# Performance work log

Measured on AMD Instinct MI355X. Metric: run time of the kernel, lower is better.

Reference implementation:

```python
import jax, jax.numpy as jnp
import numpy as np

B, S, IN_DIM, LATENT, SYM = 16, 256, 512, 512, 128
NUM_NODES, NUM_CODES, MAX_OPS, MAX_BUS = 4, 512, 4, 32
HALT_EPS, MAX_SEQ = 1e-3, 256


def setup_inputs() -> dict:
    key = jax.random.key(0)
    ks = jax.random.split(key, 10)

    def lin(k, out_d, in_d, pre=()):
        kw, kb = jax.random.split(k)
        lim = 1.0 / np.sqrt(in_d).astype(np.float32)
        w = jax.random.uniform(kw, pre + (out_d, in_d), minval=-lim, maxval=lim, dtype=jnp.float32)
        b = jax.random.uniform(kb, pre + (out_d,), minval=-lim, maxval=lim, dtype=jnp.float32)
        return w, b

    x = jax.random.normal(ks[0], (B, S, IN_DIM), jnp.float32)
    ipw, ipb = lin(ks[1], LATENT, IN_DIM)
    tp = jax.random.normal(ks[2], (1, MAX_SEQ, LATENT), jnp.float32)
    N = (NUM_NODES,)
    sw, sb = lin(ks[3], SYM, LATENT, N)
    qw, qb = lin(ks[4], 1, SYM, N)
    rw, rb = lin(ks[5], LATENT, 2 * LATENT, N)
    c1w, c1b = lin(ks[6], LATENT, LATENT + SYM, N)
    c2w, c2b = lin(ks[7], LATENT, LATENT, N)
    cb = jax.random.normal(ks[8], (NUM_NODES, NUM_CODES, SYM), jnp.float32)
    return {"x": x, "input_proj_w": ipw, "input_proj_b": ipb, "token_prompts": tp,
            "sym_w": sw, "sym_b": sb, "qry_w": qw, "qry_b": qb,
            "read_w": rw, "read_b": rb, "c1_w": c1w, "c1_b": c1b,
            "c2_w": c2w, "c2_b": c2b, "codebook": cb}


def _forward(x, input_proj_w, input_proj_b, token_prompts, sym_w, sym_b, qry_w, qry_b,
             read_w, read_b, c1_w, c1_b, c2_w, c2_b, codebook):
    Bx, Sx, _ = x.shape
    N = Bx * Sx
    # input projection + positional prompts
    out = jnp.einsum('bsi,li->bsl', x, input_proj_w) + input_proj_b + token_prompts[:, :Sx, :]
    prev_out = out
    active = jnp.ones((Bx, Sx), bool)
    token_tags = jnp.zeros((Bx, Sx, SYM), x.dtype)
    # TensorBus rolling buffers ([max_bus, B, S, dim]); with default cfg the roll branch never fires
    sym_buf = jnp.zeros((MAX_BUS, Bx, Sx, SYM), x.dtype)          # slot 0 = zero tags (initial append)
    out_buf = jnp.zeros((MAX_BUS, Bx, Sx, LATENT), x.dtype).at[0].set(out)
    msg_mask = jnp.zeros((MAX_BUS,), bool).at[0].set(True)
    ptr = 1  # static python int: appends are a fixed unrolled schedule (1 + MAX_OPS*NUM_NODES <= MAX_BUS)
    slot_ids = jnp.arange(MAX_BUS)

    for t in range(MAX_OPS):
        # snapshot of active messages for this op step (get_active)
        snap_active = msg_mask & (slot_ids < ptr)                  # [MAX_BUS]
        syms_flat = sym_buf.reshape(MAX_BUS, N, SYM)
        outs_flat = out_buf.reshape(MAX_BUS, N, LATENT)
        keep_all = jnp.ones((MAX_BUS,), bool)
        for n in range(NUM_NODES):
            # relevance of each bus message per token; inactive slots masked out of argmax
            rel = jnp.einsum('tnd,d->tn', syms_flat, qry_w[n, 0]) + qry_b[n, 0]
            rel = jnp.where(snap_active[:, None], rel, jnp.asarray(-1e9, rel.dtype))
            top = jnp.argmax(rel, axis=0)                          # [N] chosen message per token
            chosen = jnp.take_along_axis(outs_flat, top[None, :, None], axis=0)[0]  # [N, LATENT]
            bus_ctx = chosen.reshape(Bx, Sx, LATENT)
            z = jnp.concatenate([out, bus_ctx], axis=-1)
            z_read = jnp.einsum('bsk,lk->bsl', z, read_w[n]) + read_b[n]
            raw_sym = jnp.einsum('bsl,dl->bsd', z_read, sym_w[n]) + sym_b[n]
            # EMA quantizer (eval): nearest codebook entry by euclidean distance
            flat = raw_sym.reshape(-1, SYM)
            cbn = codebook[n]
            d2 = (jnp.sum(flat * flat, axis=-1, keepdims=True)
                  - 2.0 * flat @ cbn.T + jnp.sum(cbn * cbn, axis=-1))
            idx = jnp.argmin(d2, axis=-1)
            quant = cbn[idx].reshape(Bx, Sx, SYM)
            h = jnp.concatenate([z_read, quant], axis=-1)
            hid = jax.nn.relu(jnp.einsum('bsk,lk->bsl', h, c1_w[n]) + c1_b[n])
            node_out = jnp.einsum('bsl,ol->bso', hid, c2_w[n]) + c2_b[n] + out
            # halting / selective update
            delta = jnp.linalg.norm(node_out - prev_out, axis=-1)
            halt = (delta < HALT_EPS) & active
            assigned = active if t > 0 else jnp.ones_like(active)
            upd = assigned & jnp.logical_not(halt)
            out = jnp.where(upd[..., None], node_out, out)
            token_tags = jnp.where(upd[..., None], quant, token_tags)
            # bus.append
            sym_buf = sym_buf.at[ptr].set(quant)
            out_buf = out_buf.at[ptr].set(node_out)
            msg_mask = msg_mask.at[ptr].set(True)
            ptr += 1
            # keep_mask: messages never selected by any token stay alive
            counts = jnp.zeros((MAX_BUS,), jnp.int32).at[top].add(1)
            keep_all = keep_all & (counts == 0)
            active = active & jnp.logical_not(halt)
            prev_out = out
        # mark_consumed: ones over valid slots ANDed with per-node keep masks at snapshot-active
        # slots (inactive/new slots get True -> faithful to the torch init_global_mask quirk)
        msg_mask = (slot_ids < ptr) & keep_all
    return out


def reference(x, input_proj_w, input_proj_b, token_prompts, sym_w, sym_b, qry_w, qry_b,
              read_w, read_b, c1_w, c1_b, c2_w, c2_b, codebook):
    return _forward(x, input_proj_w, input_proj_b, token_prompts, sym_w, sym_b, qry_w, qry_b,
                    read_w, read_b, c1_w, c1_b, c2_w, c2_b, codebook)
```

## Files before the change

### kernel.cpp

```cpp
#include <hip/hip_runtime.h>
#include <math.h>

namespace {

typedef _Float16 f16;
typedef __attribute__((ext_vector_type(8))) _Float16 f16x8;
typedef __attribute__((ext_vector_type(4))) float f32x4;

constexpr int TOK = 4096;
constexpr int DL  = 512;
constexpr int DS  = 128;
constexpr int NC  = 512;
constexpr int NSLOT = 13;

__device__ __forceinline__ float wsum(float v){
  #pragma unroll
  for(int o=32;o>0;o>>=1) v += __shfl_xor(v,o);
  return v;
}

__device__ __forceinline__ void gload16(const void* g, void* l){
  __builtin_amdgcn_global_load_lds(
      (const __attribute__((address_space(1))) unsigned int*)g,
      (__attribute__((address_space(3))) unsigned int*)l, 16, 0, 0);
}

__device__ __forceinline__ int slotb(int row, int g){
  return (((row ^ ((row>>2)&1))<<2) | (g ^ (row&3))) << 4;
}

template<int AMODE,int EPI>
__global__ __launch_bounds__(256,2) void mgemm(
    const f16* __restrict__ A1h, const f16* __restrict__ A1l,
    const f16* __restrict__ A2h, const f16* __restrict__ A2l,
    const int* __restrict__ gidx,
    const f16* __restrict__ Bh, const f16* __restrict__ Bl,
    const float* __restrict__ bias, const float* __restrict__ res,
    float* __restrict__ Cf, f16* __restrict__ Ch, f16* __restrict__ Cl,
    f16* __restrict__ C2h, f16* __restrict__ C2l,
    int K, int K0)
{
  constexpr int SMB = 16384;
  __shared__ __align__(16) char smem[2*SMB];
  const int tid = threadIdx.x, w = tid>>6, l = tid&63;
  const int m0 = blockIdx.x*64, n0 = blockIdx.y*64;
  const int NK = K>>5, SW = K0>>5;

  const f16* sp[4]; const f16* sp2[4]; int loff[4];
  #pragma unroll
  for(int i=0;i<4;i++){
    int c = 4*w+i;
    int isA = (c<8);
    int plane = isA ? (c>>2) : ((c-8)>>2);
    int cidx  = isA ? (c&3)  : ((c-8)&3);
    loff[i] = (isA?0:8192) + plane*4096 + cidx*1024;
    int s = (cidx<<6) + l;
    int rp = s>>2, row = rp ^ ((rp>>2)&1), g = (s&3) ^ (row&3);
    int g8 = g<<3;
    if(isA){
      int m = m0 + row;
      const f16* p1 = (plane? A1l : A1h) + ((size_t)m<<9) + g8;
      sp[i] = p1;
      if(AMODE==1)      sp2[i] = (plane? A2l : A2h) + ((size_t)gidx[m]<<21) + ((size_t)m<<9) + g8;
      else if(AMODE==2) sp2[i] = (plane? A2l : A2h) + ((size_t)gidx[m]<<7) + g8;
      else              sp2[i] = p1;
    } else {
      sp[i] = (plane? Bl : Bh) + (size_t)(n0+row)*K + g8;
      sp2[i] = sp[i];
    }
  }

  const int wr = w>>1, wc = w&1, q = l>>4, r = l&15;
  int aoff[2], boff[2];
  #pragma unroll
  for(int i=0;i<2;i++) aoff[i] = slotb(32*wr + 16*i + r, q);
  #pragma unroll
  for(int j=0;j<2;j++) boff[j] = 8192 + slotb(32*wc + 16*j + r, q);

  f32x4 acc1[2][2] = {}, acc2[2][2] = {};

  #pragma unroll
  for(int i=0;i<4;i++) gload16(sp[i], smem + loff[i]);
  __syncthreads();

  int buf = 0;
  for(int kt=0; kt<NK; ++kt){
    if(kt+1 < NK){
      int nb = buf^1;
      #pragma unroll
      for(int i=0;i<4;i++){
        if(AMODE!=0 && (4*w+i)<8 && (kt+1)==SW) sp[i] = sp2[i];
        else                                     sp[i] += 32;
        gload16(sp[i], smem + nb*SMB + loff[i]);
      }
    }
    const char* Lb = smem + buf*SMB;
    f16x8 ah[2], al[2], bh[2], bl[2];
    #pragma unroll
    for(int i=0;i<2;i++){
      ah[i] = *(const f16x8*)(Lb + aoff[i]);
      al[i] = *(const f16x8*)(Lb + 4096 + aoff[i]);
    }
    #pragma unroll
    for(int j=0;j<2;j++){
      bh[j] = *(const f16x8*)(Lb + boff[j]);
      bl[j] = *(const f16x8*)(Lb + 4096 + boff[j]);
    }
    #pragma unroll
    for(int i=0;i<2;i++)
      #pragma unroll
      for(int j=0;j<2;j++){
        acc1[i][j] = __builtin_amdgcn_mfma_f32_16x16x32_f16(ah[i], bh[j], acc1[i][j], 0,0,0);
        acc2[i][j] = __builtin_amdgcn_mfma_f32_16x16x32_f16(ah[i], bl[j], acc2[i][j], 0,0,0);
        acc2[i][j] = __builtin_amdgcn_mfma_f32_16x16x32_f16(al[i], bh[j], acc2[i][j], 0,0,0);
      }
    __syncthreads();
    buf ^= 1;
  }

  #pragma unroll
  for(int i=0;i<2;i++)
    #pragma unroll
    for(int j=0;j<2;j++)
      #pragma unroll
      for(int rr=0;rr<4;rr++){
        int rowm = m0 + 32*wr + 16*i + 4*q + rr;
        int coln = n0 + 32*wc + 16*j + r;
        size_t o = ((size_t)rowm<<9) + coln;
        float v = acc1[i][j][rr] + acc2[i][j][rr]*(1.0f/2048.0f) + bias[coln];
        if(EPI==2) v = fmaxf(v, 0.f);
        if(EPI==3) v += res[o];
        if(EPI==4) v += res[(((size_t)(rowm&255))<<9) + coln];
        if(EPI==1 || EPI==3 || EPI==4) Cf[o] = v;
        if(EPI==0 || EPI==2 || EPI==4){
          f16 h = (f16)v;
          Ch[o] = h; Cl[o] = (f16)((v-(float)h)*2048.0f);
        }
        if(EPI==4){
          f16 h = (f16)v;
          C2h[o] = h; C2l[o] = (f16)((v-(float)h)*2048.0f);
        }
      }
}

__global__ void split_k(const float* __restrict__ src, f16* __restrict__ hi,
                        f16* __restrict__ lo, int n){
  for(int i = blockIdx.x*256 + threadIdx.x; i < n; i += gridDim.x*256){
    float v = src[i];
    f16 h = (f16)v;
    hi[i] = h;
    lo[i] = (f16)((v - (float)h)*2048.0f);
  }
}

__global__ __launch_bounds__(256)
void wcomb_k(const float* __restrict__ A, const float* __restrict__ Wall,
             float* __restrict__ C)
{
  constexpr int T=256;
  __shared__ float As[32][68];
  __shared__ float Ws[32][132];
  const int tid = threadIdx.x;
  const int m0 = blockIdx.x*64, n0 = blockIdx.y*128;
  const float* W = Wall + (size_t)(m0>>9)*DS*DL;
  const int ty = tid>>4, tx = tid&15;
  float4 pa[2], pw[4];
  auto loadA = [&](int k0){
    #pragma unroll
    for(int it=0; it<2; ++it){
      int v = tid + T*it; int rr = v>>3, c4 = v&7;
      pa[it] = *(const float4*)(A + (size_t)(m0+rr)*DS + k0 + (c4<<2));
    }
  };
  auto loadW = [&](int k0){
    #pragma unroll
    for(int it=0; it<4; ++it){
      int v = tid + T*it; int rr = v>>5, c4 = v&31;
      pw[it] = *(const float4*)(W + (size_t)(k0+rr)*DL + n0 + (c4<<2));
    }
  };
  float acc[4][8];
  #pragma unroll
  for(int i=0;i<4;i++)
    #pragma unroll
    for(int j=0;j<8;j++) acc[i][j]=0.f;
  loadA(0); loadW(0);
  for(int k0=0; k0<DS; k0+=32){
    __syncthreads();
    #pragma unroll
    for(int it=0; it<2; ++it){
      int v = tid + T*it; int rr=v>>3, c4=v&7;
      As[(c4<<2)+0][rr]=pa[it].x; As[(c4<<2)+1][rr]=pa[it].y;
      As[(c4<<2)+2][rr]=pa[it].z; As[(c4<<2)+3][rr]=pa[it].w;
    }
    #pragma unroll
    for(int it=0; it<4; ++it){
      int v = tid + T*it; int rr=v>>5, c4=v&31;
      *(float4*)&Ws[rr][c4<<2] = pw[it];
    }
    __syncthreads();
    if(k0+32 < DS){ loadA(k0+32); loadW(k0+32); }
    #pragma unroll
    for(int kk=0; kk<32; kk++){
      float4 a4 = *(const float4*)&As[kk][ty<<2];
      float4 b0 = *(const float4*)&Ws[kk][tx<<2];
      float4 b1 = *(const float4*)&Ws[kk][64+(tx<<2)];
      float a[4]={a4.x,a4.y,a4.z,a4.w};
      float b[8]={b0.x,b0.y,b0.z,b0.w,b1.x,b1.y,b1.z,b1.w};
      #pragma unroll
      for(int i=0;i<4;i++)
        #pragma unroll
        for(int j=0;j<8;j++) acc[i][j] = fmaf(a[i], b[j], acc[i][j]);
    }
  }
  #pragma unroll
  for(int i=0;i<4;i++){
    int m = m0 + (ty<<2) + i;
    #pragma unroll
    for(int j=0;j<8;j++){
      int n = n0 + ((j<4)? (tx<<2)+j : 64+(tx<<2)+(j-4));
      C[((size_t)m<<9)+n] = acc[i][j];
    }
  }
}

__global__ void init_k(int* __restrict__ msg, int* __restrict__ act,
                       float* __restrict__ relc, const float* __restrict__ qb,
                       int* __restrict__ cons){
  int i = blockIdx.x*256 + threadIdx.x;
  if(i < TOK){
    act[i] = 1;
    #pragma unroll
    for(int nn=0;nn<4;nn++) relc[nn*TOK + i] = qb[nn];
  }
  if(i < 32){ msg[i] = (i==0) ? 1 : 0; cons[i] = 0; }
}

__global__ void bias2_k(const float* __restrict__ cb, const float* __restrict__ sb,
                        float* __restrict__ b2){
  int row = blockIdx.x*4 + (threadIdx.x>>6);
  int lane = threadIdx.x&63;
  const float* cv = cb + ((size_t)row<<7);
  const float* sbn = sb + ((row>>9)<<7);
  float c0=cv[lane], c1=cv[lane+64];
  float nrm = c0*c0 + c1*c1;
  float dt  = c0*sbn[lane] + c1*sbn[lane+64];
  nrm = wsum(nrm); dt = wsum(dt);
  if(lane==0) b2[row] = dt - 0.5f*nrm;
}

__global__ void relmax_k(const float* __restrict__ relc, const int* __restrict__ msg,
                         int pt, int node, int* __restrict__ top, int* __restrict__ cons){
  int tok = blockIdx.x*256 + threadIdx.x;
  float best = -1e9f; int bs = 0;
  for(int s=0;s<pt;s++){
    float v = msg[s] ? relc[(size_t)((s<<2)+node)*TOK + tok] : -1e9f;
    if(v > best){ best = v; bs = s; }
  }
  top[tok] = bs;
  cons[bs] = 1;
}

__global__ void codemax_k(const float* __restrict__ sc, int* __restrict__ idx){
  int m = blockIdx.x*4 + (threadIdx.x>>6);
  int lane = threadIdx.x&63;
  const float* row = sc + ((size_t)m<<9);
  float best = -INFINITY; int bi = 0;
  #pragma unroll
  for(int rr=0;rr<8;rr++){
    int c = lane + (rr<<6);
    float v = row[c];
    if(v > best){ best=v; bi=c; }
  }
  #pragma unroll
  for(int o=32;o>0;o>>=1){
    float ov = __shfl_xor(best,o);
    int   oi = __shfl_xor(bi,o);
    if(ov > best || (ov==best && oi<bi)){ best=ov; bi=oi; }
  }
  if(lane==0) idx[m]=bi;
}

__global__ void mupdate_k(const float* __restrict__ no_, float* __restrict__ out,
                          f16* __restrict__ outh, f16* __restrict__ outl,
                          f16* __restrict__ slabh, f16* __restrict__ slabl,
                          float* __restrict__ relc, const int* __restrict__ idx,
                          const float* __restrict__ cbn, const float* __restrict__ qw,
                          const float* __restrict__ qb, int* __restrict__ act,
                          int* __restrict__ cons, int* __restrict__ msg,
                          int t, int ptr, int pe){
  int m = blockIdx.x*4 + (threadIdx.x>>6);
  int lane = threadIdx.x&63;
  const float* nrow = no_ + ((size_t)m<<9);
  float* orow = out + ((size_t)m<<9);
  float nv[8]; float s=0.f;
  #pragma unroll
  for(int rr=0;rr<8;rr++){
    int c = lane + (rr<<6);
    nv[rr]=nrow[c];
    float d = nv[rr]-orow[c]; s += d*d;
  }
  s = wsum(s);
  float delta = sqrtf(s);
  int a = act[m];
  int halt = (delta < 1e-3f) && a;
  int assigned = (t>0) ? a : 1;
  int upd = assigned && !halt;
  if(lane==0) act[m] = a && !halt;
  if(upd){
    #pragma unroll
    for(int rr=0;rr<8;rr++){
      int c = lane + (rr<<6);
      float v = nv[rr];
      orow[c] = v;
      f16 h = (f16)v;
      outh[((size_t)m<<9)+c] = h;
      outl[((size_t)m<<9)+c] = (f16)((v-(float)h)*2048.0f);
    }
  }
  if(ptr >= 0){
    size_t so = (((size_t)ptr)<<21) + ((size_t)m<<9);
    #pragma unroll
    for(int rr=0;rr<8;rr++){
      int c = lane + (rr<<6);
      float v = nv[rr];
      f16 h = (f16)v;
      slabh[so+c] = h;
      slabl[so+c] = (f16)((v-(float)h)*2048.0f);
    }
    const float* qv = cbn + ((size_t)idx[m]<<7);
    float q0=qv[lane], q1=qv[lane+64];
    #pragma unroll
    for(int nn=0;nn<4;nn++){
      float pr = q0*qw[(nn<<7)+lane] + q1*qw[(nn<<7)+64+lane];
      pr = wsum(pr);
      if(lane==0) relc[(size_t)((ptr<<2)+nn)*TOK + m] = pr + qb[nn];
    }
  }
  if(pe >= 0 && blockIdx.x==0 && threadIdx.x < 32){
    int s2 = threadIdx.x;
    msg[s2] = (s2 < pe) && !cons[s2];
    cons[s2] = 0;
  }
}

}

extern "C" void kernel_launch(void* const* d_in, const int* in_sizes, int n_in,
                              void* d_out, int out_size, void* d_ws, size_t ws_size,
                              hipStream_t stream)
{
  (void)in_sizes; (void)n_in; (void)out_size; (void)ws_size;
  const float* x   = (const float*)d_in[0];
  const float* ipw = (const float*)d_in[1];
  const float* ipb = (const float*)d_in[2];
  const float* tp  = (const float*)d_in[3];
  const float* sw  = (const float*)d_in[4];
  const float* sb  = (const float*)d_in[5];
  const float* qw  = (const float*)d_in[6];
  const float* qb  = (const float*)d_in[7];
  const float* rw  = (const float*)d_in[8];
  const float* rb  = (const float*)d_in[9];
  const float* c1w = (const float*)d_in[10];
  const float* c1b = (const float*)d_in[11];
  const float* c2w = (const float*)d_in[12];
  const float* c2b = (const float*)d_in[13];
  const float* cb  = (const float*)d_in[14];
  float* out = (float*)d_out;

  char* p = (char*)d_ws;
  auto alloc = [&](size_t b)->char*{ char* r=p; p += (b+255)&~(size_t)255; return r; };
  f16* slabh = (f16*)alloc((size_t)NSLOT*TOK*DL*2);
  f16* slabl = (f16*)alloc((size_t)NSLOT*TOK*DL*2);
  f16* outh  = (f16*)alloc((size_t)TOK*DL*2);
  f16* outl  = (f16*)alloc((size_t)TOK*DL*2);
  f16* zh    = (f16*)alloc((size_t)TOK*DL*2);
  f16* zl    = (f16*)alloc((size_t)TOK*DL*2);
  f16* hh    = (f16*)alloc((size_t)TOK*DL*2);
  f16* hl    = (f16*)alloc((size_t)TOK*DL*2);
  float* sn  = (float*)alloc((size_t)TOK*DL*4);
  f16* rwh   = (f16*)alloc((size_t)4*DL*1024*2);
  f16* rwl   = (f16*)alloc((size_t)4*DL*1024*2);
  f16* c1h   = (f16*)alloc((size_t)4*DL*640*2);
  f16* c1l   = (f16*)alloc((size_t)4*DL*640*2);
  f16* c2h   = (f16*)alloc((size_t)4*DL*DL*2);
  f16* c2l   = (f16*)alloc((size_t)4*DL*DL*2);
  f16* wch   = (f16*)alloc((size_t)4*NC*DL*2);
  f16* wcl   = (f16*)alloc((size_t)4*NC*DL*2);
  f16* iph   = (f16*)alloc((size_t)DL*DL*2);
  f16* ipl   = (f16*)alloc((size_t)DL*DL*2);
  f16* cbh   = (f16*)alloc((size_t)4*NC*DS*2);
  f16* cbl   = (f16*)alloc((size_t)4*NC*DS*2);
  float* b2  = (float*)alloc(4*NC*4);
  float* relc= (float*)alloc((size_t)NSLOT*4*TOK*4);
  int* top   = (int*)alloc(TOK*4);
  int* idxb  = (int*)alloc(TOK*4);
  int* act   = (int*)alloc(TOK*4);
  int* msg   = (int*)alloc(256);
  int* cons  = (int*)alloc(256);

  dim3 G(64,8), B(256);

  init_k<<<16,256,0,stream>>>(msg, act, relc, qb, cons);
  bias2_k<<<512,256,0,stream>>>(cb, sb, b2);
  wcomb_k<<<dim3(32,4),B,0,stream>>>(cb, sw, sn);
  split_k<<<2048,256,0,stream>>>(x,   hh,  hl,  TOK*DL);
  split_k<<<512 ,256,0,stream>>>(ipw, iph, ipl, DL*DL);
  split_k<<<2048,256,0,stream>>>(rw,  rwh, rwl, 4*DL*1024);
  split_k<<<2048,256,0,stream>>>(c1w, c1h, c1l, 4*DL*640);
  split_k<<<1024,256,0,stream>>>(c2w, c2h, c2l, 4*DL*DL);
  split_k<<<512 ,256,0,stream>>>(cb,  cbh, cbl, 4*NC*DS);
  split_k<<<1024,256,0,stream>>>(sn,  wch, wcl, 4*NC*DL);

  mgemm<0,4><<<G,B,0,stream>>>(hh,hl, nullptr,nullptr, nullptr, iph,ipl,
      ipb, tp, out, outh,outl, slabh,slabl, DL, DL);

  int ptr = 1;
  for(int t=0;t<4;t++){
    int pt = 1 + 4*t;
    for(int n=0;n<4;n++){
      relmax_k<<<16,256,0,stream>>>(relc, msg, pt, n, top, cons);
      mgemm<1,0><<<G,B,0,stream>>>(outh,outl, slabh,slabl, top,
          rwh+(size_t)n*DL*1024, rwl+(size_t)n*DL*1024, rb+(size_t)n*DL,
          nullptr, nullptr, zh,zl, nullptr,nullptr, 1024, 512);
      mgemm<0,1><<<G,B,0,stream>>>(zh,zl, nullptr,nullptr, nullptr,
          wch+(size_t)n*NC*DL, wcl+(size_t)n*NC*DL, b2+(size_t)n*NC,
          nullptr, sn, nullptr,nullptr, nullptr,nullptr, 512, 512);
      codemax_k<<<1024,256,0,stream>>>(sn, idxb);
      mgemm<2,2><<<G,B,0,stream>>>(zh,zl, cbh+(size_t)n*NC*DS, cbl+(size_t)n*NC*DS, idxb,
          c1h+(size_t)n*DL*640, c1l+(size_t)n*DL*640, c1b+(size_t)n*DL,
          nullptr, nullptr, hh,hl, nullptr,nullptr, 640, 512);
      mgemm<0,3><<<G,B,0,stream>>>(hh,hl, nullptr,nullptr, nullptr,
          c2h+(size_t)n*DL*DL, c2l+(size_t)n*DL*DL, c2b+(size_t)n*DL,
          out, sn, nullptr,nullptr, nullptr,nullptr, 512, 512);
      mupdate_k<<<1024,256,0,stream>>>(sn, out, outh,outl, slabh,slabl, relc, idxb,
          cb+(size_t)n*NC*DS, qw, qb, act, cons, msg, t,
          (t<3)? ptr : -1, (n==3 && t<3)? (1+4*(t+1)) : -1);
      ptr++;
    }
  }
}
```

Baseline: 1.321 ms.

## Fuse codebook argmax into score GEMM epilogue and triple-buffer GEMM loads

The score GEMM no longer writes the full 4096x512 fp32 score matrix. Its epilogue now reduces each 64-column tile to a per-row partial argmax, and the following c1 GEMM combines the eight partials into the final code index. This removes the separate codemax kernel and the score matrix round trip through memory. Separately, the GEMM mainloop moves from double to triple buffering with explicit vmcnt waits, so loads stay two tiles ahead. That triples LDS to 48KB per block, which may lower occupancy under launch_bounds(256,2).

```diff
diff --git a/kernel.cpp b/kernel.cpp
--- a/kernel.cpp
+++ b/kernel.cpp
@@ -38,13 +38,32 @@
     const float* __restrict__ bias, const float* __restrict__ res,
     float* __restrict__ Cf, f16* __restrict__ Ch, f16* __restrict__ Cl,
     f16* __restrict__ C2h, f16* __restrict__ C2l,
+    float* __restrict__ scpv, int* __restrict__ scpi, int* __restrict__ idxg,
     int K, int K0)
 {
   constexpr int SMB = 16384;
-  __shared__ __align__(16) char smem[2*SMB];
+  __shared__ __align__(16) char smem[3*SMB];
+  __shared__ int gsel[64];
+  __shared__ float redv[4][32];
+  __shared__ int   redi[4][32];
   const int tid = threadIdx.x, w = tid>>6, l = tid&63;
   const int m0 = blockIdx.x*64, n0 = blockIdx.y*64;
   const int NK = K>>5, SW = K0>>5;
+
+  if(AMODE==2){
+    if(tid<64){
+      int m = m0+tid;
+      float bv = -INFINITY; int bi = 0;
+      #pragma unroll
+      for(int y=0;y<8;y++){
+        float v = scpv[(size_t)y*TOK + m];
+        if(v > bv){ bv=v; bi=scpi[(size_t)y*TOK + m]; }
+      }
+      gsel[tid]=bi;
+      idxg[m]=bi;
+    }
+    __syncthreads();
+  }
 
   const f16* sp[4]; const f16* sp2[4]; int loff[4];
   #pragma unroll
@@ -62,7 +81,7 @@
       const f16* p1 = (plane? A1l : A1h) + ((size_t)m<<9) + g8;
       sp[i] = p1;
       if(AMODE==1)      sp2[i] = (plane? A2l : A2h) + ((size_t)gidx[m]<<21) + ((size_t)m<<9) + g8;
-      else if(AMODE==2) sp2[i] = (plane? A2l : A2h) + ((size_t)gidx[m]<<7) + g8;
+      else if(AMODE==2) sp2[i] = (plane? A2l : A2h) + ((size_t)gsel[row]<<7) + g8;
       else              sp2[i] = p1;
     } else {
       sp[i] = (plane? Bl : Bh) + (size_t)(n0+row)*K + g8;
@@ -79,22 +98,26 @@
 
   f32x4 acc1[2][2] = {}, acc2[2][2] = {};
 
+  auto advance = [&](int snext){
+    #pragma unroll
+    for(int i=0;i<4;i++){
+      if(AMODE!=0 && (4*w+i)<8 && snext==SW) sp[i] = sp2[i];
+      else                                    sp[i] += 32;
+    }
+  };
+
   #pragma unroll
   for(int i=0;i<4;i++) gload16(sp[i], smem + loff[i]);
-  __syncthreads();
-
-  int buf = 0;
+  advance(1);
+  #pragma unroll
+  for(int i=0;i<4;i++) gload16(sp[i], smem + SMB + loff[i]);
+  advance(2);
+  asm volatile("s_waitcnt vmcnt(4)" ::: "memory");
+  __builtin_amdgcn_s_barrier();
+
+  int roff = 0, soff = 2*SMB;
   for(int kt=0; kt<NK; ++kt){
-    if(kt+1 < NK){
-      int nb = buf^1;
-      #pragma unroll
-      for(int i=0;i<4;i++){
-        if(AMODE!=0 && (4*w+i)<8 && (kt+1)==SW) sp[i] = sp2[i];
-        else                                     sp[i] += 32;
-        gload16(sp[i], smem + nb*SMB + loff[i]);
-      }
-    }
-    const char* Lb = smem + buf*SMB;
+    const char* Lb = smem + roff;
     f16x8 ah[2], al[2], bh[2], bl[2];
     #pragma unroll
     for(int i=0;i<2;i++){
@@ -105,6 +128,11 @@
     for(int j=0;j<2;j++){
       bh[j] = *(const f16x8*)(Lb + boff[j]);
       bl[j] = *(const f16x8*)(Lb + 4096 + boff[j]);
+    }
+    if(kt+2 < NK){
+      #pragma unroll
+      for(int i=0;i<4;i++) gload16(sp[i], smem + soff + loff[i]);
+      advance(kt+3);
     }
     #pragma unroll
     for(int i=0;i<2;i++)
@@ -114,33 +142,67 @@
         acc2[i][j] = __builtin_amdgcn_mfma_f32_16x16x32_f16(ah[i], bl[j], acc2[i][j], 0,0,0);
         acc2[i][j] = __builtin_amdgcn_mfma_f32_16x16x32_f16(al[i], bh[j], acc2[i][j], 0,0,0);
       }
+    if(kt+2 < NK){
+      asm volatile("s_waitcnt vmcnt(4)" ::: "memory");
+      __builtin_amdgcn_s_barrier();
+    } else if(kt+1 < NK){
+      asm volatile("s_waitcnt vmcnt(0)" ::: "memory");
+      __builtin_amdgcn_s_barrier();
+    }
+    roff = (roff==2*SMB)? 0 : roff+SMB;
+    soff = (soff==2*SMB)? 0 : soff+SMB;
+  }
+
+  if(EPI!=1){
+    #pragma unroll
+    for(int i=0;i<2;i++)
+      #pragma unroll
+      for(int j=0;j<2;j++)
+        #pragma unroll
+        for(int rr=0;rr<4;rr++){
+          int rowm = m0 + 32*wr + 16*i + 4*q + rr;
+          int coln = n0 + 32*wc + 16*j + r;
+          size_t o = ((size_t)rowm<<9) + coln;
+          float v = acc1[i][j][rr] + acc2[i][j][rr]*(1.0f/2048.0f) + bias[coln];
+          if(EPI==2) v = fmaxf(v, 0.f);
+          if(EPI==3) v += res[o];
+          if(EPI==4) v += res[(((size_t)(rowm&255))<<9) + coln];
+          if(EPI==3 || EPI==4) Cf[o] = v;
+          if(EPI==0 || EPI==2 || EPI==4){
+            f16 h = (f16)v;
+            Ch[o] = h; Cl[o] = (f16)((v-(float)h)*2048.0f);
+          }
+          if(EPI==4){
+            f16 h = (f16)v;
+            C2h[o] = h; C2l[o] = (f16)((v-(float)h)*2048.0f);
+          }
+        }
+  } else {
+    #pragma unroll
+    for(int i=0;i<2;i++)
+      #pragma unroll
+      for(int rr=0;rr<4;rr++){
+        float v0 = acc1[i][0][rr] + acc2[i][0][rr]*(1.0f/2048.0f) + bias[n0+32*wc+r];
+        float v1 = acc1[i][1][rr] + acc2[i][1][rr]*(1.0f/2048.0f) + bias[n0+32*wc+16+r];
+        float bv; int bc;
+        if(v1 > v0){ bv=v1; bc=n0+32*wc+16+r; } else { bv=v0; bc=n0+32*wc+r; }
+        #pragma unroll
+        for(int o=1;o<16;o<<=1){
+          float ov = __shfl_xor(bv,o); int oi = __shfl_xor(bc,o);
+          if(ov>bv || (ov==bv && oi<bc)){ bv=ov; bc=oi; }
+        }
+        if(r==0){ redv[w][16*i+4*q+rr]=bv; redi[w][16*i+4*q+rr]=bc; }
+      }
     __syncthreads();
-    buf ^= 1;
-  }
-
-  #pragma unroll
-  for(int i=0;i<2;i++)
-    #pragma unroll
-    for(int j=0;j<2;j++)
-      #pragma unroll
-      for(int rr=0;rr<4;rr++){
-        int rowm = m0 + 32*wr + 16*i + 4*q + rr;
-        int coln = n0 + 32*wc + 16*j + r;
-        size_t o = ((size_t)rowm<<9) + coln;
-        float v = acc1[i][j][rr] + acc2[i][j][rr]*(1.0f/2048.0f) + bias[coln];
-        if(EPI==2) v = fmaxf(v, 0.f);
-        if(EPI==3) v += res[o];
-        if(EPI==4) v += res[(((size_t)(rowm&255))<<9) + coln];
-        if(EPI==1 || EPI==3 || EPI==4) Cf[o] = v;
-        if(EPI==0 || EPI==2 || EPI==4){
-          f16 h = (f16)v;
-          Ch[o] = h; Cl[o] = (f16)((v-(float)h)*2048.0f);
-        }
-        if(EPI==4){
-          f16 h = (f16)v;
-          C2h[o] = h; C2l[o] = (f16)((v-(float)h)*2048.0f);
-        }
-      }
+    if(tid<64){
+      int wr2 = tid>>5, li = tid&31;
+      float bv = redv[2*wr2][li]; int bc = redi[2*wr2][li];
+      float ov = redv[2*wr2+1][li]; int oi = redi[2*wr2+1][li];
+      if(ov>bv || (ov==bv && oi<bc)){ bv=ov; bc=oi; }
+      scpv[(size_t)blockIdx.y*TOK + m0 + tid] = bv;
+      scpi[(size_t)blockIdx.y*TOK + m0 + tid] = bc;
+    }
+  }
 }
 
 __global__ void split_k(const float* __restrict__ src, f16* __restrict__ hi,
@@ -259,26 +321,6 @@
   }
   top[tok] = bs;
   cons[bs] = 1;
-}
-
-__global__ void codemax_k(const float* __restrict__ sc, int* __restrict__ idx){
-  int m = blockIdx.x*4 + (threadIdx.x>>6);
-  int lane = threadIdx.x&63;
-  const float* row = sc + ((size_t)m<<9);
-  float best = -INFINITY; int bi = 0;
-  #pragma unroll
-  for(int rr=0;rr<8;rr++){
-    int c = lane + (rr<<6);
-    float v = row[c];
-    if(v > best){ best=v; bi=c; }
-  }
-  #pragma unroll
-  for(int o=32;o>0;o>>=1){
-    float ov = __shfl_xor(best,o);
-    int   oi = __shfl_xor(bi,o);
-    if(ov > best || (ov==best && oi<bi)){ best=ov; bi=oi; }
-  }
-  if(lane==0) idx[m]=bi;
 }
 
 __global__ void mupdate_k(const float* __restrict__ no_, float* __restrict__ out,
@@ -393,6 +435,8 @@
   f16* cbl   = (f16*)alloc((size_t)4*NC*DS*2);
   float* b2  = (float*)alloc(4*NC*4);
   float* relc= (float*)alloc((size_t)NSLOT*4*TOK*4);
+  float* scpv= (float*)alloc((size_t)8*TOK*4);
+  int* scpi  = (int*)alloc((size_t)8*TOK*4);
   int* top   = (int*)alloc(TOK*4);
   int* idxb  = (int*)alloc(TOK*4);
   int* act   = (int*)alloc(TOK*4);
@@ -413,7 +457,7 @@
   split_k<<<1024,256,0,stream>>>(sn,  wch, wcl, 4*NC*DL);
 
   mgemm<0,4><<<G,B,0,stream>>>(hh,hl, nullptr,nullptr, nullptr, iph,ipl,
-      ipb, tp, out, outh,outl, slabh,slabl, DL, DL);
+      ipb, tp, out, outh,outl, slabh,slabl, nullptr,nullptr,nullptr, DL, DL);
 
   int ptr = 1;
   for(int t=0;t<4;t++){
@@ -422,17 +466,16 @@
       relmax_k<<<16,256,0,stream>>>(relc, msg, pt, n, top, cons);
       mgemm<1,0><<<G,B,0,stream>>>(outh,outl, slabh,slabl, top,
           rwh+(size_t)n*DL*1024, rwl+(size_t)n*DL*1024, rb+(size_t)n*DL,
-          nullptr, nullptr, zh,zl, nullptr,nullptr, 1024, 512);
+          nullptr, nullptr, zh,zl, nullptr,nullptr, nullptr,nullptr,nullptr, 1024, 512);
       mgemm<0,1><<<G,B,0,stream>>>(zh,zl, nullptr,nullptr, nullptr,
           wch+(size_t)n*NC*DL, wcl+(size_t)n*NC*DL, b2+(size_t)n*NC,
-          nullptr, sn, nullptr,nullptr, nullptr,nullptr, 512, 512);
-      codemax_k<<<1024,256,0,stream>>>(sn, idxb);
-      mgemm<2,2><<<G,B,0,stream>>>(zh,zl, cbh+(size_t)n*NC*DS, cbl+(size_t)n*NC*DS, idxb,
+          nullptr, nullptr, nullptr,nullptr, nullptr,nullptr, scpv,scpi,nullptr, 512, 512);
+      mgemm<2,2><<<G,B,0,stream>>>(zh,zl, cbh+(size_t)n*NC*DS, cbl+(size_t)n*NC*DS, nullptr,
           c1h+(size_t)n*DL*640, c1l+(size_t)n*DL*640, c1b+(size_t)n*DL,
-          nullptr, nullptr, hh,hl, nullptr,nullptr, 640, 512);
+          nullptr, nullptr, hh,hl, nullptr,nullptr, scpv,scpi,idxb, 640, 512);
       mgemm<0,3><<<G,B,0,stream>>>(hh,hl, nullptr,nullptr, nullptr,
           c2h+(size_t)n*DL*DL, c2l+(size_t)n*DL*DL, c2b+(size_t)n*DL,
-          out, sn, nullptr,nullptr, nullptr,nullptr, 512, 512);
+          out, sn, nullptr,nullptr, nullptr,nullptr, nullptr,nullptr,nullptr, 512, 512);
       mupdate_k<<<1024,256,0,stream>>>(sn, out, outh,outl, slabh,slabl, relc, idxb,
           cb+(size_t)n*NC*DS, qw, qb, act, cons, msg, t,
           (t<3)? ptr : -1, (n==3 && t<3)? (1+4*(t+1)) : -1);
```

New measurement: 1.305 ms. Within noise of the previous version (-1.2%).
